# Kernel tuning notes

Measured on AMD Instinct MI355X. Metric: run time of the kernel, lower is better.

Reference implementation:

```python
import jax, jax.numpy as jnp
import numpy as np

EPS = 1e-5

def _bn(x, gamma, beta, mean, var):
    # eval-mode BatchNorm2d
    inv = gamma / jnp.sqrt(var + EPS)
    return x * inv[None, :, None, None] + (beta - mean * inv)[None, :, None, None]

def _conv(x, w):
    # Conv2d kernel 3x3, padding=(1,0), no bias; width already circularly padded
    return jax.lax.conv_general_dilated(x, w, (1, 1), [(1, 1), (0, 0)],
                                        dimension_numbers=('NCHW', 'OIHW', 'NCHW'))

def _circ_pad_w(x):
    # F.pad(x, (1,1,0,0), mode='circular')
    return jnp.pad(x, ((0, 0), (0, 0), (0, 0), (1, 1)), mode='wrap')

def _forward(flow_matrix, polar_fea, range_fea,
             fusion_w, fusion_gamma, fusion_beta, fusion_mean, fusion_var,
             attn_w, attn_gamma, attn_beta, attn_mean, attn_var):
    N, C, Hr, Wr = range_fea.shape
    _, _, H, W = polar_fea.shape
    _, h, w, K, _ = flow_matrix.shape
    # nearest-resize flow grid to (H, W) (identity when h==H, w==W)
    ri = jnp.arange(H) * h // H
    ci = jnp.arange(W) * w // W
    flow = flow_matrix[:, ri][:, :, ci]                       # [N,H,W,K,2]
    # torch.flip(dims=[-1]) then pad z=0: grid x=flow[...,1], y=flow[...,0], z=0.
    # Din=1 and z=0 with align_corners=False => iz=0 exactly -> pure 2D bilinear.
    gx = flow[..., 1]
    gy = flow[..., 0]
    ix = ((gx + 1.0) * Wr - 1.0) * 0.5                        # [N,H,W,K]
    iy = ((gy + 1.0) * Hr - 1.0) * 0.5
    feat_flat = range_fea.reshape(N, C, Hr * Wr)

    def gather(yi, xi):
        # yi, xi: [N,H,W] int32; zeros padding outside
        valid = (yi >= 0) & (yi < Hr) & (xi >= 0) & (xi < Wr)
        lin = jnp.clip(yi, 0, Hr - 1) * Wr + jnp.clip(xi, 0, Wr - 1)
        v = jax.vmap(lambda f, l: jnp.take(f, l.reshape(-1), axis=1))(feat_flat, lin)
        v = v.reshape(N, C, H, W)
        return v * valid[:, None].astype(v.dtype)

    def step(carry, grid_k):
        ixk, iyk = grid_k                                     # [N,H,W]
        x0 = jnp.floor(ixk); y0 = jnp.floor(iyk)
        wx1 = ixk - x0;      wy1 = iyk - y0
        x0i = x0.astype(jnp.int32); y0i = y0.astype(jnp.int32)
        val = (((1 - wy1) * (1 - wx1))[:, None] * gather(y0i,     x0i)
             + ((1 - wy1) * wx1)[:, None]       * gather(y0i,     x0i + 1)
             + (wy1 * (1 - wx1))[:, None]       * gather(y0i + 1, x0i)
             + (wy1 * wx1)[:, None]             * gather(y0i + 1, x0i + 1))
        return jnp.maximum(carry, val), None

    init = jnp.full((N, C, H, W), -jnp.inf, range_fea.dtype)
    grids = (jnp.moveaxis(ix, -1, 0), jnp.moveaxis(iy, -1, 0))  # [K,N,H,W]
    flow_fea, _ = jax.lax.scan(step, init, grids)               # max over K samples

    fea = jnp.concatenate([polar_fea, flow_fea], axis=1)        # [N,2C,H,W]
    res = _conv(_circ_pad_w(fea), fusion_w)
    res = jax.nn.relu(_bn(res, fusion_gamma, fusion_beta, fusion_mean, fusion_var))
    att = _conv(_circ_pad_w(res), attn_w)
    att = jax.nn.softmax(_bn(att, attn_gamma, attn_beta, attn_mean, attn_var), axis=1)
    return polar_fea + res * att


def setup_inputs() -> dict:
    key = jax.random.key(0)
    ks = jax.random.split(key, 6)
    N, C, H, W, K, Hr, Wr = 1, 64, 480, 360, 32, 64, 2048
    flow_matrix = jax.random.uniform(ks[0], (N, H, W, K, 2), jnp.float32, -1.0, 1.0)
    polar_fea = jax.random.normal(ks[1], (N, C, H, W), jnp.float32)
    range_fea = jax.random.normal(ks[2], (N, C, Hr, Wr), jnp.float32)
    fusion_w = jax.random.normal(ks[3], (C, 2 * C, 3, 3), jnp.float32) * 0.02
    attn_w = jax.random.normal(ks[4], (C, C, 3, 3), jnp.float32) * 0.02
    ones = jnp.ones((C,), jnp.float32)
    zeros = jnp.zeros((C,), jnp.float32)
    return {
        'flow_matrix': flow_matrix, 'polar_fea': polar_fea, 'range_fea': range_fea,
        'fusion_w': fusion_w, 'fusion_gamma': ones, 'fusion_beta': zeros,
        'fusion_mean': zeros, 'fusion_var': ones,
        'attn_w': attn_w, 'attn_gamma': ones, 'attn_beta': zeros,
        'attn_mean': zeros, 'attn_var': ones,
    }


def reference(flow_matrix, polar_fea, range_fea,
              fusion_w, fusion_gamma, fusion_beta, fusion_mean, fusion_var,
              attn_w, attn_gamma, attn_beta, attn_mean, attn_var):
    return _forward(flow_matrix, polar_fea, range_fea,
                    fusion_w, fusion_gamma, fusion_beta, fusion_mean, fusion_var,
                    attn_w, attn_gamma, attn_beta, attn_mean, attn_var)
```

## Files before the change

kernel.cpp:

```cpp
#include <hip/hip_runtime.h>
#include <math.h>

#define CCH 64
#define HH 480
#define WW 360
#define KK 32
#define HR 64
#define WR 2048
#define NPIX (HH*WW)
#define RFNPIX (HR*WR)
#define ZOFF 16777216u
#define NEGOFF 16777344u

typedef __attribute__((ext_vector_type(8))) short short8;
typedef __attribute__((ext_vector_type(4))) float f32x4;
typedef __attribute__((ext_vector_type(4))) int  int4_;

__device__ __forceinline__ ushort f2bf(float f) {
    uint u = __float_as_uint(f);
    return (ushort)((u + 0x7fffu + ((u >> 16) & 1u)) >> 16);
}

__global__ __launch_bounds__(256) void k_wprep(const float* __restrict__ fw,
                                               const float* __restrict__ aw,
                                               ushort* __restrict__ wA1,
                                               ushort* __restrict__ wA2) {
    int t = blockIdx.x * 256 + threadIdx.x;
    if (t < 73728) {
        int j = t & 7, ln = (t >> 3) & 63, Mf = (t >> 9) & 3, rem = t >> 11;
        int tap = rem % 9, c = rem / 9;
        int o = Mf * 16 + (ln & 15);
        int ci = c * 32 + ((ln >> 4) & 3) * 8 + j;
        wA1[t] = f2bf(fw[(o * 128 + ci) * 9 + tap]);
    } else if (t < 73728 + 36864) {
        int i = t - 73728;
        int j = i & 7, ln = (i >> 3) & 63, Mf = (i >> 9) & 3, rem = i >> 11;
        int tap = rem % 9, c = rem / 9;
        int o = Mf * 16 + (ln & 15);
        int ci = c * 32 + ((ln >> 4) & 3) * 8 + j;
        wA2[i] = f2bf(aw[(o * 64 + ci) * 9 + tap]);
    }
}

__global__ __launch_bounds__(256) void k_tr(const float* __restrict__ src,
                                            ushort* __restrict__ dst,
                                            int npix, int rowShorts) {
    __shared__ float lds[64][65];
    int t = threadIdx.x;
    int pix0 = blockIdx.x * 64;
    int lx = t & 63, ty = t >> 6;
    #pragma unroll
    for (int cc = 0; cc < 64; cc += 4) {
        int c = cc + ty;
        lds[c][lx] = src[(size_t)c * npix + pix0 + lx];
    }
    __syncthreads();
    int cp = t & 31, po = t >> 5;
    #pragma unroll
    for (int pl = po; pl < 64; pl += 8) {
        uint u = (uint)f2bf(lds[2 * cp][pl]) | ((uint)f2bf(lds[2 * cp + 1][pl]) << 16);
        *(uint*)(dst + (size_t)(pix0 + pl) * rowShorts + cp * 2) = u;
    }
}

__global__ void k_zero(uint* __restrict__ rft32) {
    int t = threadIdx.x;
    if (t < 32)       rft32[(ZOFF >> 2) + t] = 0;
    else if (t < 64)  rft32[(NEGOFF >> 2) + (t - 32)] = 0xFF7FFF7Fu;
}

__global__ __launch_bounds__(256) void k_sample(const float* __restrict__ flow,
                                                const char* __restrict__ rftb,
                                                ushort* __restrict__ xin) {
    __shared__ __align__(16) uint pbuf[4][2][33][8];
    int tid = threadIdx.x;
    int ln = tid & 63;
    int wid = tid >> 6;
    int half = ln >> 5;
    int gwave = blockIdx.x * 4 + wid;

    int k = ln & 31;
    int pix = gwave * 2 + half;
    const float* fp = flow + (size_t)pix * 64 + 2 * k;
    float gy = fp[0], gx = fp[1];
    float ix = fmaf(gx, 1024.f, 1023.5f);
    float iy = fmaf(gy, 32.f, 31.5f);
    float xf = floorf(ix), yf = floorf(iy);
    float wx = ix - xf, wy = iy - yf;
    int x0 = (int)xf, y0 = (int)yf;
    bool xv0 = (unsigned)x0 < (unsigned)WR;
    bool xv1 = (unsigned)(x0 + 1) < (unsigned)WR;
    bool yv0 = (unsigned)y0 < (unsigned)HR;
    bool yv1 = (unsigned)(y0 + 1) < (unsigned)HR;
    int xc0 = x0 < 0 ? 0 : x0;
    int xc1 = x0 + 1 > WR - 1 ? WR - 1 : x0 + 1;
    int yc0 = y0 < 0 ? 0 : y0;
    int yc1 = y0 + 1 > HR - 1 ? HR - 1 : y0 + 1;
    uint o00 = (xv0 && yv0) ? (uint)(((yc0 << 11) + xc0) << 7) : ZOFF;
    uint o01 = (xv1 && yv0) ? (uint)(((yc0 << 11) + xc1) << 7) : ZOFF;
    uint o10 = (xv0 && yv1) ? (uint)(((yc1 << 11) + xc0) << 7) : ZOFF;
    uint o11 = (xv1 && yv1) ? (uint)(((yc1 << 11) + xc1) << 7) : ZOFF;
    float w00 = (1.f - wy) * (1.f - wx);
    float w01 = (1.f - wy) * wx;
    float w10 = wy * (1.f - wx);
    float w11 = wy * wx;

    int sid = yc0 >> 4;
    unsigned long long b0 = __ballot(sid == 0);
    unsigned long long b1 = __ballot(sid == 1);
    unsigned long long b2 = __ballot(sid == 2);
    unsigned long long b3 = __ballot(sid == 3);
    unsigned long long hm = half ? 0xFFFFFFFF00000000ull : 0x00000000FFFFFFFFull;
    int c0 = __popcll(b0 & hm), c1 = __popcll(b1 & hm);
    int c2 = __popcll(b2 & hm), c3 = __popcll(b3 & hm);
    int st1 = c0, st2 = c0 + c1, st3 = c0 + c1 + c2;
    unsigned long long mysel = (sid == 0) ? b0 : (sid == 1) ? b1 : (sid == 2) ? b2 : b3;
    unsigned long long lower = (1ull << ln) - 1ull;
    int rank = __popcll(mysel & hm & lower);
    int mystart = (sid == 0) ? 0 : (sid == 1) ? st1 : (sid == 2) ? st2 : st3;
    int pos = mystart + rank;
    *(int4_*)&pbuf[wid][half][pos][0] =
        (int4_){(int)o00, __float_as_int(w00), (int)o01, __float_as_int(w01)};
    *(int4_*)&pbuf[wid][half][pos][4] =
        (int4_){(int)o10, __float_as_int(w10), (int)o11, __float_as_int(w11)};
    if ((ln & 31) == 0) {
        *(int4_*)&pbuf[wid][half][32][0] =
            (int4_){(int)NEGOFF, __float_as_int(1.0f), (int)ZOFF, 0};
        *(int4_*)&pbuf[wid][half][32][4] = (int4_){(int)ZOFF, 0, (int)ZOFF, 0};
    }
    __syncthreads();

    uint laneByte = (uint)((ln & 31) * 4);
    const uint* pb = &pbuf[wid][half][0][0];
    float mLo = -3.0e38f, mHi = -3.0e38f;
    int cnts[4]  = {c0, c1, c2, c3};
    int starts[4] = {0, st1, st2, st3};

    #pragma unroll
    for (int s = 0; s < 4; s++) {
        int myCnt = cnts[s];
        int myStart = starts[s];
        int cA = __builtin_amdgcn_readlane(myCnt, 0);
        int cB = __builtin_amdgcn_readlane(myCnt, 32);
        int trip = cA > cB ? cA : cB;
        for (int i = 0; i < trip; i++) {
            int idx = (i < myCnt) ? (myStart + i) : 32;
            const uint* e = pb + idx * 8;
            uint2 e0 = *(const uint2*)(e + 0);
            uint2 e1 = *(const uint2*)(e + 2);
            uint2 e2 = *(const uint2*)(e + 4);
            uint2 e3 = *(const uint2*)(e + 6);
            uint d0 = *(const uint*)(rftb + (e0.x + laneByte));
            uint d1 = *(const uint*)(rftb + (e1.x + laneByte));
            uint d2 = *(const uint*)(rftb + (e2.x + laneByte));
            uint d3 = *(const uint*)(rftb + (e3.x + laneByte));
            float W0 = __uint_as_float(e0.y);
            float W1 = __uint_as_float(e1.y);
            float W2 = __uint_as_float(e2.y);
            float W3 = __uint_as_float(e3.y);

            float vlo = W0 * __uint_as_float(d0 << 16);
            vlo = fmaf(W1, __uint_as_float(d1 << 16), vlo);
            vlo = fmaf(W2, __uint_as_float(d2 << 16), vlo);
            vlo = fmaf(W3, __uint_as_float(d3 << 16), vlo);
            float vhi = W0 * __uint_as_float(d0 & 0xffff0000u);
            vhi = fmaf(W1, __uint_as_float(d1 & 0xffff0000u), vhi);
            vhi = fmaf(W2, __uint_as_float(d2 & 0xffff0000u), vhi);
            vhi = fmaf(W3, __uint_as_float(d3 & 0xffff0000u), vhi);
            mLo = fmaxf(mLo, vlo);
            mHi = fmaxf(mHi, vhi);
        }
    }

    uint outw;
    asm("v_cvt_pk_bf16_f32 %0, %1, %2" : "=v"(outw) : "v"(mLo), "v"(mHi));
    *(uint*)((char*)xin + (size_t)pix * 256 + 128 + (ln & 31) * 4) = outw;
}

__global__ __launch_bounds__(256) void k_mconv1(const ushort* __restrict__ xin,
                                                const ushort* __restrict__ wA,
                                                const float* __restrict__ g,
                                                const float* __restrict__ b,
                                                const float* __restrict__ mn,
                                                const float* __restrict__ vr,
                                                float* __restrict__ res_t) {
    __shared__ __align__(16) ushort xt[3][194][32];
    int tid = threadIdx.x;
    int h = blockIdx.x >> 1, w0 = (blockIdx.x & 1) * 180;
    int wid = tid >> 6, ln = tid & 63;
    f32x4 acc[4][3];
    #pragma unroll
    for (int m = 0; m < 4; m++)
        #pragma unroll
        for (int nf = 0; nf < 3; nf++) acc[m][nf] = (f32x4){0.f, 0.f, 0.f, 0.f};

    for (int c = 0; c < 4; c++) {
        __syncthreads();
        for (int i = tid; i < 2184; i += 256) {
            int q = i & 3, s = i >> 2;
            int r = s / 182, pw = s - r * 182;
            int gh = h + r - 1;
            int gw = w0 + pw - 1;
            if (gw < 0) gw += WW;
            if (gw >= WW) gw -= WW;
            int4_ val = {0, 0, 0, 0};
            if ((unsigned)gh < (unsigned)HH)
                val = *(const int4_*)(xin + ((size_t)(gh * WW + gw) * 128 + c * 32 + q * 8));
            *(int4_*)&xt[r][pw][(q ^ (pw & 3)) * 8] = val;
        }
        __syncthreads();
        #pragma unroll
        for (int tap = 0; tap < 9; tap++) {
            int dh = tap / 3, dw = tap % 3;
            short8 aF[4];
            #pragma unroll
            for (int m = 0; m < 4; m++)
                aF[m] = *(const short8*)(wA + (size_t)(((c * 9 + tap) * 4 + m) * 64 + ln) * 8);
            short8 bF[3];
            #pragma unroll
            for (int nf = 0; nf < 3; nf++) {
                int pw = wid * 48 + nf * 16 + (ln & 15) + dw;
                bF[nf] = *(const short8*)&xt[dh][pw][((((ln >> 4) & 3)) ^ (pw & 3)) * 8];
            }
            #pragma unroll
            for (int m = 0; m < 4; m++)
                #pragma unroll
                for (int nf = 0; nf < 3; nf++)
                    acc[m][nf] = __builtin_amdgcn_mfma_f32_16x16x32_bf16(aF[m], bF[nf], acc[m][nf], 0, 0, 0);
        }
    }
    #pragma unroll
    for (int m = 0; m < 4; m++) {
        #pragma unroll
        for (int reg = 0; reg < 4; reg++) {
            int o = m * 16 + ((ln >> 4) & 3) * 4 + reg;
            float sc = g[o] * rsqrtf(vr[o] + 1e-5f);
            float bi = b[o] - mn[o] * sc;
            #pragma unroll
            for (int nf = 0; nf < 3; nf++) {
                int n = wid * 48 + nf * 16 + (ln & 15);
                if (n < 180) {
                    int P = h * WW + w0 + n;
                    float v = fmaf(acc[m][nf][reg], sc, bi);
                    res_t[(size_t)P * 64 + o] = fmaxf(v, 0.f);
                }
            }
        }
    }
}

__global__ __launch_bounds__(256) void k_mconv2(const float* __restrict__ res_t,
                                                const float* __restrict__ polar,
                                                const ushort* __restrict__ wA,
                                                const float* __restrict__ g,
                                                const float* __restrict__ b,
                                                const float* __restrict__ mn,
                                                const float* __restrict__ vr,
                                                float* __restrict__ out) {
    __shared__ __align__(16) ushort xt[3][194][32];
    int tid = threadIdx.x;
    int h = blockIdx.x >> 1, w0 = (blockIdx.x & 1) * 180;
    int wid = tid >> 6, ln = tid & 63;
    f32x4 acc[4][3];
    #pragma unroll
    for (int m = 0; m < 4; m++)
        #pragma unroll
        for (int nf = 0; nf < 3; nf++) acc[m][nf] = (f32x4){0.f, 0.f, 0.f, 0.f};

    for (int c = 0; c < 2; c++) {
        __syncthreads();
        for (int i = tid; i < 2184; i += 256) {
            int q = i & 3, s = i >> 2;
            int r = s / 182, pw = s - r * 182;
            int gh = h + r - 1;
            int gw = w0 + pw - 1;
            if (gw < 0) gw += WW;
            if (gw >= WW) gw -= WW;
            int4_ val = {0, 0, 0, 0};
            if ((unsigned)gh < (unsigned)HH) {
                const float* src = res_t + ((size_t)(gh * WW + gw) * 64 + c * 32 + q * 8);
                f32x4 va = *(const f32x4*)src;
                f32x4 vb = *(const f32x4*)(src + 4);
                uint u0, u1, u2, u3;
                asm("v_cvt_pk_bf16_f32 %0, %1, %2" : "=v"(u0) : "v"(va[0]), "v"(va[1]));
                asm("v_cvt_pk_bf16_f32 %0, %1, %2" : "=v"(u1) : "v"(va[2]), "v"(va[3]));
                asm("v_cvt_pk_bf16_f32 %0, %1, %2" : "=v"(u2) : "v"(vb[0]), "v"(vb[1]));
                asm("v_cvt_pk_bf16_f32 %0, %1, %2" : "=v"(u3) : "v"(vb[2]), "v"(vb[3]));
                val = (int4_){(int)u0, (int)u1, (int)u2, (int)u3};
            }
            *(int4_*)&xt[r][pw][(q ^ (pw & 3)) * 8] = val;
        }
        __syncthreads();
        #pragma unroll
        for (int tap = 0; tap < 9; tap++) {
            int dh = tap / 3, dw = tap % 3;
            short8 aF[4];
            #pragma unroll
            for (int m = 0; m < 4; m++)
                aF[m] = *(const short8*)(wA + (size_t)(((c * 9 + tap) * 4 + m) * 64 + ln) * 8);
            short8 bF[3];
            #pragma unroll
            for (int nf = 0; nf < 3; nf++) {
                int pw = wid * 48 + nf * 16 + (ln & 15) + dw;
                bF[nf] = *(const short8*)&xt[dh][pw][((((ln >> 4) & 3)) ^ (pw & 3)) * 8];
            }
            #pragma unroll
            for (int m = 0; m < 4; m++)
                #pragma unroll
                for (int nf = 0; nf < 3; nf++)
                    acc[m][nf] = __builtin_amdgcn_mfma_f32_16x16x32_bf16(aF[m], bF[nf], acc[m][nf], 0, 0, 0);
        }
    }
    #pragma unroll
    for (int m = 0; m < 4; m++) {
        #pragma unroll
        for (int reg = 0; reg < 4; reg++) {
            int o = m * 16 + ((ln >> 4) & 3) * 4 + reg;
            float sc = g[o] * rsqrtf(vr[o] + 1e-5f);
            float bi = b[o] - mn[o] * sc;
            #pragma unroll
            for (int nf = 0; nf < 3; nf++)
                acc[m][nf][reg] = fmaf(acc[m][nf][reg], sc, bi);
        }
    }
    #pragma unroll
    for (int nf = 0; nf < 3; nf++) {
        float mx = -3.0e38f;
        #pragma unroll
        for (int m = 0; m < 4; m++)
            #pragma unroll
            for (int reg = 0; reg < 4; reg++) mx = fmaxf(mx, acc[m][nf][reg]);
        mx = fmaxf(mx, __shfl_xor(mx, 16));
        mx = fmaxf(mx, __shfl_xor(mx, 32));
        float s = 0.f;
        #pragma unroll
        for (int m = 0; m < 4; m++)
            #pragma unroll
            for (int reg = 0; reg < 4; reg++) {
                float e = __expf(acc[m][nf][reg] - mx);
                acc[m][nf][reg] = e;
                s += e;
            }
        s += __shfl_xor(s, 16);
        s += __shfl_xor(s, 32);
        float rinv = 1.f / s;
        int n = wid * 48 + nf * 16 + (ln & 15);
        if (n < 180) {
            int P = h * WW + w0 + n;
            #pragma unroll
            for (int m = 0; m < 4; m++)
                #pragma unroll
                for (int reg = 0; reg < 4; reg++) {
                    int o = m * 16 + ((ln >> 4) & 3) * 4 + reg;
                    float att = acc[m][nf][reg] * rinv;
                    out[(size_t)o * NPIX + P] =
                        fmaf(res_t[(size_t)P * 64 + o], att, polar[(size_t)o * NPIX + P]);
                }
        }
    }
}

extern "C" void kernel_launch(void* const* d_in, const int* in_sizes, int n_in,
                              void* d_out, int out_size, void* d_ws, size_t ws_size,
                              hipStream_t stream) {
    const float* flow  = (const float*)d_in[0];
    const float* polar = (const float*)d_in[1];
    const float* rf    = (const float*)d_in[2];
    const float* fw    = (const float*)d_in[3];
    const float* fg    = (const float*)d_in[4];
    const float* fb    = (const float*)d_in[5];
    const float* fm    = (const float*)d_in[6];
    const float* fv    = (const float*)d_in[7];
    const float* aw    = (const float*)d_in[8];
    const float* ag    = (const float*)d_in[9];
    const float* ab    = (const float*)d_in[10];
    const float* am    = (const float*)d_in[11];
    const float* av    = (const float*)d_in[12];
    float* out = (float*)d_out;

    char* wsb = (char*)d_ws;
    ushort* xin   = (ushort*)wsb;
    ushort* rft   = (ushort*)(wsb + 44236800);
    float*  res_t = (float*)(wsb + 61014272);
    ushort* wA1   = (ushort*)(wsb + 105251072);
    ushort* wA2   = wA1 + 73728;

    k_wprep<<<432, 256, 0, stream>>>(fw, aw, wA1, wA2);
    k_tr<<<NPIX / 64, 256, 0, stream>>>(polar, xin, NPIX, 128);
    k_tr<<<RFNPIX / 64, 256, 0, stream>>>(rf, rft, RFNPIX, 64);
    k_zero<<<1, 64, 0, stream>>>((uint*)rft);
    k_sample<<<NPIX / 8, 256, 0, stream>>>(flow, (const char*)rft, xin);
    k_mconv1<<<960, 256, 0, stream>>>(xin, wA1, fg, fb, fm, fv, res_t);
    k_mconv2<<<960, 256, 0, stream>>>(res_t, polar, wA2, ag, ab, am, av, out);
}
```

Baseline: 440.7 us.

## Split sampling into two row-band passes and store conv1 residual in bf16

The sampling kernel now runs twice. Each pass handles only the taps whose source row falls in one 32-row half of the range feature map, and the second pass merges by max with the first pass's output. The goal is to shrink the working set each pass gathers from so it fits in cache better, at the cost of reading flow twice and a read-modify-write of the output. The conv1 residual is also stored as bf16 instead of fp32, halving that intermediate's traffic and removing the conversion in conv2, with a small precision change in the residual term. Flow loads and sample stores use nontemporal hints.

New measurement: 364.5 us, median of 2. 1.21x faster.

```diff
diff --git a/kernel.cpp b/kernel.cpp
--- a/kernel.cpp
+++ b/kernel.cpp
@@ -71,7 +71,8 @@
 
 __global__ __launch_bounds__(256) void k_sample(const float* __restrict__ flow,
                                                 const char* __restrict__ rftb,
-                                                ushort* __restrict__ xin) {
+                                                ushort* __restrict__ xin,
+                                                int sel, int mergePrev) {
     __shared__ __align__(16) uint pbuf[4][2][33][8];
     int tid = threadIdx.x;
     int ln = tid & 63;
@@ -82,7 +83,8 @@
     int k = ln & 31;
     int pix = gwave * 2 + half;
     const float* fp = flow + (size_t)pix * 64 + 2 * k;
-    float gy = fp[0], gx = fp[1];
+    float gy = __builtin_nontemporal_load(fp);
+    float gx = __builtin_nontemporal_load(fp + 1);
     float ix = fmaf(gx, 1024.f, 1023.5f);
     float iy = fmaf(gy, 32.f, 31.5f);
     float xf = floorf(ix), yf = floorf(iy);
@@ -105,20 +107,14 @@
     float w10 = wy * (1.f - wx);
     float w11 = wy * wx;
 
-    int sid = yc0 >> 4;
-    unsigned long long b0 = __ballot(sid == 0);
-    unsigned long long b1 = __ballot(sid == 1);
-    unsigned long long b2 = __ballot(sid == 2);
-    unsigned long long b3 = __ballot(sid == 3);
+    bool isIn = ((yc0 >> 5) == sel);
     unsigned long long hm = half ? 0xFFFFFFFF00000000ull : 0x00000000FFFFFFFFull;
-    int c0 = __popcll(b0 & hm), c1 = __popcll(b1 & hm);
-    int c2 = __popcll(b2 & hm), c3 = __popcll(b3 & hm);
-    int st1 = c0, st2 = c0 + c1, st3 = c0 + c1 + c2;
-    unsigned long long mysel = (sid == 0) ? b0 : (sid == 1) ? b1 : (sid == 2) ? b2 : b3;
     unsigned long long lower = (1ull << ln) - 1ull;
-    int rank = __popcll(mysel & hm & lower);
-    int mystart = (sid == 0) ? 0 : (sid == 1) ? st1 : (sid == 2) ? st2 : st3;
-    int pos = mystart + rank;
+    unsigned long long balIn = __ballot(isIn);
+    int cntIn = __popcll(balIn & hm);
+    int rankIn = __popcll(balIn & hm & lower);
+    int rankOut = __popcll(~balIn & hm & lower);
+    int pos = isIn ? rankIn : (cntIn + rankOut);
     *(int4_*)&pbuf[wid][half][pos][0] =
         (int4_){(int)o00, __float_as_int(w00), (int)o01, __float_as_int(w01)};
     *(int4_*)&pbuf[wid][half][pos][4] =
@@ -133,48 +129,47 @@
     uint laneByte = (uint)((ln & 31) * 4);
     const uint* pb = &pbuf[wid][half][0][0];
     float mLo = -3.0e38f, mHi = -3.0e38f;
-    int cnts[4]  = {c0, c1, c2, c3};
-    int starts[4] = {0, st1, st2, st3};
-
-    #pragma unroll
-    for (int s = 0; s < 4; s++) {
-        int myCnt = cnts[s];
-        int myStart = starts[s];
-        int cA = __builtin_amdgcn_readlane(myCnt, 0);
-        int cB = __builtin_amdgcn_readlane(myCnt, 32);
-        int trip = cA > cB ? cA : cB;
-        for (int i = 0; i < trip; i++) {
-            int idx = (i < myCnt) ? (myStart + i) : 32;
-            const uint* e = pb + idx * 8;
-            uint2 e0 = *(const uint2*)(e + 0);
-            uint2 e1 = *(const uint2*)(e + 2);
-            uint2 e2 = *(const uint2*)(e + 4);
-            uint2 e3 = *(const uint2*)(e + 6);
-            uint d0 = *(const uint*)(rftb + (e0.x + laneByte));
-            uint d1 = *(const uint*)(rftb + (e1.x + laneByte));
-            uint d2 = *(const uint*)(rftb + (e2.x + laneByte));
-            uint d3 = *(const uint*)(rftb + (e3.x + laneByte));
-            float W0 = __uint_as_float(e0.y);
-            float W1 = __uint_as_float(e1.y);
-            float W2 = __uint_as_float(e2.y);
-            float W3 = __uint_as_float(e3.y);
-
-            float vlo = W0 * __uint_as_float(d0 << 16);
-            vlo = fmaf(W1, __uint_as_float(d1 << 16), vlo);
-            vlo = fmaf(W2, __uint_as_float(d2 << 16), vlo);
-            vlo = fmaf(W3, __uint_as_float(d3 << 16), vlo);
-            float vhi = W0 * __uint_as_float(d0 & 0xffff0000u);
-            vhi = fmaf(W1, __uint_as_float(d1 & 0xffff0000u), vhi);
-            vhi = fmaf(W2, __uint_as_float(d2 & 0xffff0000u), vhi);
-            vhi = fmaf(W3, __uint_as_float(d3 & 0xffff0000u), vhi);
-            mLo = fmaxf(mLo, vlo);
-            mHi = fmaxf(mHi, vhi);
-        }
-    }
-
+    int cA = __builtin_amdgcn_readlane(cntIn, 0);
+    int cB = __builtin_amdgcn_readlane(cntIn, 32);
+    int trip = cA > cB ? cA : cB;
+
+    for (int i = 0; i < trip; i++) {
+        int idx = (i < cntIn) ? i : 32;
+        const uint* e = pb + idx * 8;
+        uint2 e0 = *(const uint2*)(e + 0);
+        uint2 e1 = *(const uint2*)(e + 2);
+        uint2 e2 = *(const uint2*)(e + 4);
+        uint2 e3 = *(const uint2*)(e + 6);
+        uint d0 = *(const uint*)(rftb + (e0.x + laneByte));
+        uint d1 = *(const uint*)(rftb + (e1.x + laneByte));
+        uint d2 = *(const uint*)(rftb + (e2.x + laneByte));
+        uint d3 = *(const uint*)(rftb + (e3.x + laneByte));
+        float W0 = __uint_as_float(e0.y);
+        float W1 = __uint_as_float(e1.y);
+        float W2 = __uint_as_float(e2.y);
+        float W3 = __uint_as_float(e3.y);
+
+        float vlo = W0 * __uint_as_float(d0 << 16);
+        vlo = fmaf(W1, __uint_as_float(d1 << 16), vlo);
+        vlo = fmaf(W2, __uint_as_float(d2 << 16), vlo);
+        vlo = fmaf(W3, __uint_as_float(d3 << 16), vlo);
+        float vhi = W0 * __uint_as_float(d0 & 0xffff0000u);
+        vhi = fmaf(W1, __uint_as_float(d1 & 0xffff0000u), vhi);
+        vhi = fmaf(W2, __uint_as_float(d2 & 0xffff0000u), vhi);
+        vhi = fmaf(W3, __uint_as_float(d3 & 0xffff0000u), vhi);
+        mLo = fmaxf(mLo, vlo);
+        mHi = fmaxf(mHi, vhi);
+    }
+
+    uint* xp = (uint*)((char*)xin + (size_t)pix * 256 + 128 + (ln & 31) * 4);
+    if (mergePrev) {
+        uint cur = __builtin_nontemporal_load(xp);
+        mLo = fmaxf(mLo, __uint_as_float(cur << 16));
+        mHi = fmaxf(mHi, __uint_as_float(cur & 0xffff0000u));
+    }
     uint outw;
     asm("v_cvt_pk_bf16_f32 %0, %1, %2" : "=v"(outw) : "v"(mLo), "v"(mHi));
-    *(uint*)((char*)xin + (size_t)pix * 256 + 128 + (ln & 31) * 4) = outw;
+    __builtin_nontemporal_store(outw, xp);
 }
 
 __global__ __launch_bounds__(256) void k_mconv1(const ushort* __restrict__ xin,
@@ -183,7 +178,7 @@
                                                 const float* __restrict__ b,
                                                 const float* __restrict__ mn,
                                                 const float* __restrict__ vr,
-                                                float* __restrict__ res_t) {
+                                                ushort* __restrict__ res_bf) {
     __shared__ __align__(16) ushort xt[3][194][32];
     int tid = threadIdx.x;
     int h = blockIdx.x >> 1, w0 = (blockIdx.x & 1) * 180;
@@ -231,25 +226,35 @@
     }
     #pragma unroll
     for (int m = 0; m < 4; m++) {
-        #pragma unroll
-        for (int reg = 0; reg < 4; reg++) {
-            int o = m * 16 + ((ln >> 4) & 3) * 4 + reg;
-            float sc = g[o] * rsqrtf(vr[o] + 1e-5f);
-            float bi = b[o] - mn[o] * sc;
-            #pragma unroll
-            for (int nf = 0; nf < 3; nf++) {
-                int n = wid * 48 + nf * 16 + (ln & 15);
-                if (n < 180) {
-                    int P = h * WW + w0 + n;
-                    float v = fmaf(acc[m][nf][reg], sc, bi);
-                    res_t[(size_t)P * 64 + o] = fmaxf(v, 0.f);
-                }
+        int ob = m * 16 + ((ln >> 4) & 3) * 4;
+        float sc0 = g[ob]     * rsqrtf(vr[ob]     + 1e-5f);
+        float sc1 = g[ob + 1] * rsqrtf(vr[ob + 1] + 1e-5f);
+        float sc2 = g[ob + 2] * rsqrtf(vr[ob + 2] + 1e-5f);
+        float sc3 = g[ob + 3] * rsqrtf(vr[ob + 3] + 1e-5f);
+        float bi0 = b[ob]     - mn[ob]     * sc0;
+        float bi1 = b[ob + 1] - mn[ob + 1] * sc1;
+        float bi2 = b[ob + 2] - mn[ob + 2] * sc2;
+        float bi3 = b[ob + 3] - mn[ob + 3] * sc3;
+        #pragma unroll
+        for (int nf = 0; nf < 3; nf++) {
+            int n = wid * 48 + nf * 16 + (ln & 15);
+            if (n < 180) {
+                int P = h * WW + w0 + n;
+                float v0 = fmaxf(fmaf(acc[m][nf][0], sc0, bi0), 0.f);
+                float v1 = fmaxf(fmaf(acc[m][nf][1], sc1, bi1), 0.f);
+                float v2 = fmaxf(fmaf(acc[m][nf][2], sc2, bi2), 0.f);
+                float v3 = fmaxf(fmaf(acc[m][nf][3], sc3, bi3), 0.f);
+                uint lo, hi;
+                asm("v_cvt_pk_bf16_f32 %0, %1, %2" : "=v"(lo) : "v"(v0), "v"(v1));
+                asm("v_cvt_pk_bf16_f32 %0, %1, %2" : "=v"(hi) : "v"(v2), "v"(v3));
+                uint2 pk; pk.x = lo; pk.y = hi;
+                *(uint2*)(res_bf + (size_t)P * 64 + ob) = pk;
             }
         }
     }
 }
 
-__global__ __launch_bounds__(256) void k_mconv2(const float* __restrict__ res_t,
+__global__ __launch_bounds__(256) void k_mconv2(const ushort* __restrict__ res_bf,
                                                 const float* __restrict__ polar,
                                                 const ushort* __restrict__ wA,
                                                 const float* __restrict__ g,
@@ -277,17 +282,8 @@
             if (gw < 0) gw += WW;
             if (gw >= WW) gw -= WW;
             int4_ val = {0, 0, 0, 0};
-            if ((unsigned)gh < (unsigned)HH) {
-                const float* src = res_t + ((size_t)(gh * WW + gw) * 64 + c * 32 + q * 8);
-                f32x4 va = *(const f32x4*)src;
-                f32x4 vb = *(const f32x4*)(src + 4);
-                uint u0, u1, u2, u3;
-                asm("v_cvt_pk_bf16_f32 %0, %1, %2" : "=v"(u0) : "v"(va[0]), "v"(va[1]));
-                asm("v_cvt_pk_bf16_f32 %0, %1, %2" : "=v"(u1) : "v"(va[2]), "v"(va[3]));
-                asm("v_cvt_pk_bf16_f32 %0, %1, %2" : "=v"(u2) : "v"(vb[0]), "v"(vb[1]));
-                asm("v_cvt_pk_bf16_f32 %0, %1, %2" : "=v"(u3) : "v"(vb[2]), "v"(vb[3]));
-                val = (int4_){(int)u0, (int)u1, (int)u2, (int)u3};
-            }
+            if ((unsigned)gh < (unsigned)HH)
+                val = *(const int4_*)(res_bf + ((size_t)(gh * WW + gw) * 64 + c * 32 + q * 8));
             *(int4_*)&xt[r][pw][(q ^ (pw & 3)) * 8] = val;
         }
         __syncthreads();
@@ -353,8 +349,9 @@
                 for (int reg = 0; reg < 4; reg++) {
                     int o = m * 16 + ((ln >> 4) & 3) * 4 + reg;
                     float att = acc[m][nf][reg] * rinv;
+                    float rv = __uint_as_float((uint)res_bf[(size_t)P * 64 + o] << 16);
                     out[(size_t)o * NPIX + P] =
-                        fmaf(res_t[(size_t)P * 64 + o], att, polar[(size_t)o * NPIX + P]);
+                        fmaf(rv, att, polar[(size_t)o * NPIX + P]);
                 }
         }
     }
@@ -379,17 +376,18 @@
     float* out = (float*)d_out;
 
     char* wsb = (char*)d_ws;
-    ushort* xin   = (ushort*)wsb;
-    ushort* rft   = (ushort*)(wsb + 44236800);
-    float*  res_t = (float*)(wsb + 61014272);
-    ushort* wA1   = (ushort*)(wsb + 105251072);
-    ushort* wA2   = wA1 + 73728;
+    ushort* xin    = (ushort*)wsb;
+    ushort* rft    = (ushort*)(wsb + 44236800);
+    ushort* res_bf = (ushort*)(wsb + 61014272);
+    ushort* wA1    = (ushort*)(wsb + 83132672);
+    ushort* wA2    = wA1 + 73728;
 
     k_wprep<<<432, 256, 0, stream>>>(fw, aw, wA1, wA2);
     k_tr<<<NPIX / 64, 256, 0, stream>>>(polar, xin, NPIX, 128);
     k_tr<<<RFNPIX / 64, 256, 0, stream>>>(rf, rft, RFNPIX, 64);
     k_zero<<<1, 64, 0, stream>>>((uint*)rft);
-    k_sample<<<NPIX / 8, 256, 0, stream>>>(flow, (const char*)rft, xin);
-    k_mconv1<<<960, 256, 0, stream>>>(xin, wA1, fg, fb, fm, fv, res_t);
-    k_mconv2<<<960, 256, 0, stream>>>(res_t, polar, wA2, ag, ab, am, av, out);
-}
+    k_sample<<<NPIX / 8, 256, 0, stream>>>(flow, (const char*)rft, xin, 0, 0);
+    k_sample<<<NPIX / 8, 256, 0, stream>>>(flow, (const char*)rft, xin, 1, 1);
+    k_mconv1<<<960, 256, 0, stream>>>(xin, wA1, fg, fb, fm, fv, res_bf);
+    k_mconv2<<<960, 256, 0, stream>>>(res_bf, polar, wA2, ag, ab, am, av, out);
+}
```
